# Optimization experiments

Measured on AMD Instinct MI355X. Metric: run time of the kernel, lower is better.

## Reference

```python
import jax, jax.numpy as jnp
import numpy as np

IMG = 1280
STRIDES = (8, 16, 32)
ALPHA, GAMMA = 0.25, 2.0
OBJ_W, BOX_W, FOOT_W = 1.0, 5.0, 1.0
RADIUS, NUM_CAND, EPS = 2.5, 10, 1e-7


def _grid(H, W):
    ys, xs = jnp.meshgrid(jnp.arange(H, dtype=jnp.float32),
                          jnp.arange(W, dtype=jnp.float32), indexing='ij')
    return xs.reshape(-1), ys.reshape(-1)


def _iou_xyxy(a, b):
    lt = jnp.maximum(a[..., :2], b[..., :2])
    rb = jnp.minimum(a[..., 2:], b[..., 2:])
    wh = jnp.clip(rb - lt, 0.0)
    inter = wh[..., 0] * wh[..., 1]
    aa = (a[..., 2] - a[..., 0]) * (a[..., 3] - a[..., 1])
    ab = (b[..., 2] - b[..., 0]) * (b[..., 3] - b[..., 1])
    return inter / (aa + ab - inter + EPS)


def _assign_one(pred, gt_boxes, gt_foots, gt_valid, stride):
    # Faithful SimOTAAssigner.assign for one image/scale (torch @no_grad).
    pred = jax.lax.stop_gradient(pred)
    gt_boxes = jax.lax.stop_gradient(gt_boxes)
    gt_foots = jax.lax.stop_gradient(gt_foots)
    C, H, W = pred.shape
    HW = H * W
    gx, gy = _grid(H, W)
    s = stride / IMG
    p = pred.reshape(C, HW)
    obj_logit = p[0]
    pcx = (jax.nn.sigmoid(p[1]) + gx) * s
    pcy = (jax.nn.sigmoid(p[2]) + gy) * s
    pw = jnp.exp(jnp.clip(p[3], -5.0, 5.0)) * s
    ph = jnp.exp(jnp.clip(p[4], -5.0, 5.0)) * s
    pred_xyxy = jnp.stack([pcx - pw / 2, pcy - ph / 2, pcx + pw / 2, pcy + ph / 2], -1)
    cls_cost = jax.nn.softplus(-obj_logit)  # BCE_with_logits(logit, 1)
    cell = jnp.arange(HW)

    def step(carry, gt):
        obj_t, box_t, foot_t, pos_m = carry
        box, foot, valid = gt
        cx, cy, w, h = box[0], box[1], box[2], box[3]
        cxg, cyg = cx / s, cy / s
        in_center = (jnp.abs(gx - cxg) < RADIUS) & (jnp.abs(gy - cyg) < RADIUS)
        in_box = ((gx >= (cx - w / 2) / s) & (gx < (cx + w / 2) / s) &
                  (gy >= (cy - h / 2) / s) & (gy < (cy + h / 2) / s))
        cand = in_center | in_box
        dist = (gx - cxg) ** 2 + (gy - cyg) ** 2
        cand = jnp.where(jnp.any(cand), cand, cell == jnp.argmin(dist))
        gt_xyxy = jnp.stack([cx - w / 2, cy - h / 2, cx + w / 2, cy + h / 2])
        iou = _iou_xyxy(pred_xyxy, gt_xyxy)  # (HW,)
        cost = jnp.where(cand, cls_cost - 3.0 * jnp.log(iou + EPS), jnp.inf)
        n_cand = jnp.sum(cand)
        iou_sum = jnp.sum(jnp.where(cand, iou, 0.0))
        n_pos = jnp.clip(jnp.floor(iou_sum).astype(jnp.int32), 1,
                         jnp.minimum(NUM_CAND, n_cand))
        _, idx = jax.lax.top_k(-cost, NUM_CAND)
        sel = (jnp.arange(NUM_CAND) < n_pos) & valid
        best_iou = iou[idx[0]]  # pair_iou[topk_idx[0]] in the torch code
        pos_m = pos_m.at[idx].max(sel.astype(jnp.float32))
        obj_t = obj_t.at[idx].max(jnp.where(sel, best_iou, -jnp.inf))
        tx = cxg - gx[idx]
        ty = cyg - gy[idx]
        tw = jnp.log(w / s + EPS)
        th = jnp.log(h / s + EPS)
        new_box = jnp.stack([tx, ty, jnp.full_like(tx, tw), jnp.full_like(tx, th)], 0)
        box_t = box_t.at[:, idx].set(jnp.where(sel, new_box, box_t[:, idx]))
        new_foot = jnp.stack([jnp.full_like(tx, foot[0]), jnp.full_like(tx, foot[1])], 0)
        foot_t = foot_t.at[:, idx].set(jnp.where(sel, new_foot, foot_t[:, idx]))
        return (obj_t, box_t, foot_t, pos_m), None

    init = (jnp.zeros(HW), jnp.zeros((4, HW)), jnp.zeros((2, HW)), jnp.zeros(HW))
    (obj_t, box_t, foot_t, pos_m), _ = jax.lax.scan(
        step, init, (gt_boxes, gt_foots, gt_valid))
    return obj_t, box_t, foot_t, pos_m


def _ciou(pcx, pcy, pw, ph, tcx, tcy, tw, th):
    px1, py1, px2, py2 = pcx - pw / 2, pcy - ph / 2, pcx + pw / 2, pcy + ph / 2
    tx1, ty1, tx2, ty2 = tcx - tw / 2, tcy - th / 2, tcx + tw / 2, tcy + th / 2
    iw = jnp.clip(jnp.minimum(px2, tx2) - jnp.maximum(px1, tx1), 0.0)
    ih = jnp.clip(jnp.minimum(py2, ty2) - jnp.maximum(py1, ty1), 0.0)
    inter = iw * ih
    union = pw * ph + tw * th - inter + EPS
    iou = inter / union
    rho2 = (pcx - tcx) ** 2 + (pcy - tcy) ** 2
    cw = jnp.maximum(px2, tx2) - jnp.minimum(px1, tx1)
    ch = jnp.maximum(py2, ty2) - jnp.minimum(py1, ty1)
    c2 = cw ** 2 + ch ** 2 + EPS
    v = (4.0 / jnp.pi ** 2) * (jnp.arctan(tw / (th + EPS)) - jnp.arctan(pw / (ph + EPS))) ** 2
    alpha = jax.lax.stop_gradient(v / (1.0 - iou + v + EPS))
    return iou - rho2 / c2 - alpha * v


def _loss_one(pred, gt_boxes, gt_foots, gt_valid, stride):
    obj_t, box_t, foot_t, pm = _assign_one(pred, gt_boxes, gt_foots, gt_valid, stride)
    C, H, W = pred.shape
    HW = H * W
    p = pred.reshape(C, HW)
    gx, gy = _grid(H, W)
    s = stride / IMG
    # focal loss on objectness with soft IoU targets
    x, z = p[0], obj_t
    ce = jnp.maximum(x, 0.0) - x * z + jnp.log1p(jnp.exp(-jnp.abs(x)))
    prob = jax.nn.sigmoid(x)
    p_t = prob * z + (1.0 - prob) * (1.0 - z)
    a_t = ALPHA * z + (1.0 - ALPHA) * (1.0 - z)
    obj_loss = jnp.mean(a_t * (1.0 - p_t) ** GAMMA * ce)
    npos = jnp.maximum(jnp.sum(pm), 1.0)
    # CIoU box loss at positive cells (mask instead of gather, jit-friendly)
    pcx = (jax.nn.sigmoid(p[1]) + gx) * s
    pcy = (jax.nn.sigmoid(p[2]) + gy) * s
    pw = jnp.exp(jnp.clip(p[3], -5.0, 5.0)) * s
    ph = jnp.exp(jnp.clip(p[4], -5.0, 5.0)) * s
    tcx = (box_t[0] + gx) * s
    tcy = (box_t[1] + gy) * s
    tw = jnp.exp(box_t[2]) * s
    th = jnp.exp(box_t[3]) * s
    ciou = _ciou(pcx, pcy, pw, ph, tcx, tcy, tw, th)
    box_loss = jnp.sum(pm * (1.0 - ciou)) / npos
    # smooth-L1 foot loss on sigmoid-decoded foot point
    pf = jax.nn.sigmoid(p[5:7])
    d = jnp.abs(pf - foot_t)
    sl1 = jnp.where(d < 1.0, 0.5 * d * d, d - 0.5)
    foot_loss = jnp.sum(pm * jnp.sum(sl1, 0)) / npos
    return obj_loss, box_loss, foot_loss


def _forward(pred_s0, pred_s1, pred_s2, targets):
    B = pred_s0.shape[0]
    person = targets[..., 0] == 0  # person_mask; padded rows use cls != 0
    boxes = targets[..., 1:5]
    foots = targets[..., 5:7]
    size = jnp.maximum(boxes[..., 2], boxes[..., 3]) * IMG
    scale_masks = (size < 128.0, (size >= 48.0) & (size < 288.0), size >= 128.0)
    tot_obj = tot_box = tot_foot = 0.0
    for pred, stride, sm in zip((pred_s0, pred_s1, pred_s2), STRIDES, scale_masks):
        valid = person & sm
        o, bx, f = jax.vmap(_loss_one, in_axes=(0, 0, 0, 0, None))(
            pred, boxes, foots, valid, stride)
        tot_obj = tot_obj + jnp.sum(o)
        tot_box = tot_box + jnp.sum(bx)
        tot_foot = tot_foot + jnp.sum(f)
    return (OBJ_W * tot_obj + BOX_W * tot_box + FOOT_W * tot_foot) / B


def setup_inputs() -> dict:
    key = jax.random.key(0)
    ks = jax.random.split(key, 7)
    B, N = 64, 40
    pred_s0 = jax.random.normal(ks[0], (B, 7, 160, 160), jnp.float32)
    pred_s1 = jax.random.normal(ks[1], (B, 7, 80, 80), jnp.float32)
    pred_s2 = jax.random.normal(ks[2], (B, 7, 40, 40), jnp.float32)
    cls = (jax.random.uniform(ks[3], (B, N, 1)) > 0.9).astype(jnp.float32)
    cxy = jax.random.uniform(ks[4], (B, N, 2)) * 0.8 + 0.1
    wh = jax.random.uniform(ks[5], (B, N, 2)) * 0.28 + 0.01
    ft = jax.random.uniform(ks[6], (B, N, 2))
    targets = jnp.concatenate([cls, cxy, wh, ft], -1)
    return {"pred_s0": pred_s0, "pred_s1": pred_s1, "pred_s2": pred_s2,
            "targets": targets}


def reference(pred_s0, pred_s1, pred_s2, targets):
    return _forward(pred_s0, pred_s1, pred_s2, targets)
```

## Files before the change

### kernel.cpp

```cpp
#include <hip/hip_runtime.h>
#include <math.h>

#define NBATCH 64
#define NGT    40
#define HW0    25600
#define HW1    6400
#define HW2    1600
#define NTASK  (NBATCH*3*NGT)
#define SLICE  1600
#define BPB    21
#define NBLK   (NBATCH*BPB)
#define SENT   0xFFFFFFFFFFFFFFFFull
#define FEPS   1e-7f

__device__ __forceinline__ float sigm(float x){ return 1.0f/(1.0f+expf(-x)); }

__device__ __forceinline__ unsigned fkey(float f){
  unsigned b = __float_as_uint(f);
  return (b & 0x80000000u) ? ~b : (b | 0x80000000u);
}

__device__ __forceinline__ unsigned long long shflx64(unsigned long long v, int m){
  int lo = __shfl_xor((int)(unsigned)(v & 0xFFFFFFFFull), m, 64);
  int hi = __shfl_xor((int)(unsigned)(v >> 32), m, 64);
  return (((unsigned long long)(unsigned)hi) << 32) | (unsigned)lo;
}
__device__ __forceinline__ float wredf(float v){
  #pragma unroll
  for (int o=32;o;o>>=1) v += __shfl_xor(v,o,64);
  return v;
}
__device__ __forceinline__ int wredi(int v){
  #pragma unroll
  for (int o=32;o;o>>=1) v += __shfl_xor(v,o,64);
  return v;
}
__device__ __forceinline__ unsigned long long wredmin64(unsigned long long v){
  #pragma unroll
  for (int o=32;o;o>>=1){ unsigned long long w = shflx64(v,o); v = (w<v)?w:v; }
  return v;
}

__device__ __forceinline__ float iou_of_cell(const float* __restrict__ P, int HW, int cell,
                                             int W, float s,
                                             float bx1, float by1, float bx2, float by2, float ab){
  int gy = cell / W;
  int gx = cell - gy*W;
  float gxf=(float)gx, gyf=(float)gy;
  float q1 = P[HW+cell], q2=P[2*HW+cell], q3=P[3*HW+cell], q4=P[4*HW+cell];
  float pcx = (sigm(q1)+gxf)*s;
  float pcy = (sigm(q2)+gyf)*s;
  float pw = expf(fminf(fmaxf(q3,-5.0f),5.0f))*s;
  float ph = expf(fminf(fmaxf(q4,-5.0f),5.0f))*s;
  float ax1=pcx-pw*0.5f, ay1=pcy-ph*0.5f, ax2=pcx+pw*0.5f, ay2=pcy+ph*0.5f;
  float ltx=fmaxf(ax1,bx1), lty=fmaxf(ay1,by1);
  float rbx=fminf(ax2,bx2), rby=fminf(ay2,by2);
  float iw=fmaxf(rbx-ltx,0.0f), ih=fmaxf(rby-lty,0.0f);
  float inter=iw*ih;
  float aa=(ax2-ax1)*(ay2-ay1);
  return inter/(aa+ab-inter+FEPS);
}

__global__ __launch_bounds__(256) void k_assign(
    const float* __restrict__ p0, const float* __restrict__ p1,
    const float* __restrict__ p2, const float* __restrict__ tg,
    int2* __restrict__ meta, int* __restrict__ cells)
{
  int lane = threadIdx.x & 63;
  int task = ((blockIdx.x<<8) + threadIdx.x) >> 6;
  int g  = task % NGT;
  int bs = task / NGT;
  int sc = bs % 3;
  int b  = bs / 3;

  const float* tp = tg + (b*NGT + g)*7;
  float cls = tp[0], cx = tp[1], cy = tp[2], w = tp[3], h = tp[4];
  float sz = fmaxf(w,h)*1280.0f;
  bool valid = (cls == 0.0f);
  if (sc==0)      valid = valid && (sz < 128.0f);
  else if (sc==1) valid = valid && (sz >= 48.0f) && (sz < 288.0f);
  else            valid = valid && (sz >= 128.0f);
  if (!valid){ if (lane==0) meta[task] = make_int2(0,0); return; }

  int W, HW; float s; const float* P;
  if (sc==0)      { W=160; HW=HW0; s=8.0f/1280.0f;  P=p0; }
  else if (sc==1) { W=80;  HW=HW1; s=16.0f/1280.0f; P=p1; }
  else            { W=40;  HW=HW2; s=32.0f/1280.0f; P=p2; }
  P += (size_t)b*7*HW;

  float cxg = cx/s, cyg = cy/s;
  float bx1 = cx - w*0.5f, bx2 = cx + w*0.5f;
  float by1 = cy - h*0.5f, by2 = cy + h*0.5f;
  float ab  = (bx2-bx1)*(by2-by1);
  float bxl = bx1/s, bxr = bx2/s, byt = by1/s, byb = by2/s;

  int x0 = max(0,   (int)floorf(fminf(cxg-2.5f, bxl)) - 1);
  int x1 = min(W-1, (int)floorf(fmaxf(cxg+2.5f, bxr)) + 1);
  int y0 = max(0,   (int)floorf(fminf(cyg-2.5f, byt)) - 1);
  int y1 = min(W-1, (int)floorf(fmaxf(cyg+2.5f, byb)) + 1);
  int rw = x1-x0+1, rh = y1-y0+1;
  int rn = rw*rh;

  unsigned long long t[10];
  #pragma unroll
  for (int j=0;j<10;++j) t[j]=SENT;
  int ncand = 0; float iousum = 0.0f;
  unsigned long long dmin = SENT;

  int rx = lane % rw, ry = lane / rw;
  int stepy = 64 / rw, stepx = 64 % rw;
  for (int r = lane; r < rn; r += 64){
    float gxf = (float)(x0+rx), gyf = (float)(y0+ry);
    int cell = (y0+ry)*W + (x0+rx);
    float q1 = P[HW+cell], q2 = P[2*HW+cell], q3 = P[3*HW+cell], q4 = P[4*HW+cell];
    float pcx = (sigm(q1)+gxf)*s;
    float pcy = (sigm(q2)+gyf)*s;
    float pw = expf(fminf(fmaxf(q3,-5.0f),5.0f))*s;
    float ph = expf(fminf(fmaxf(q4,-5.0f),5.0f))*s;
    float ax1 = pcx-pw*0.5f, ay1 = pcy-ph*0.5f, ax2 = pcx+pw*0.5f, ay2 = pcy+ph*0.5f;
    float ltx = fmaxf(ax1,bx1), lty = fmaxf(ay1,by1);
    float rbx = fminf(ax2,bx2), rby = fminf(ay2,by2);
    float iw = fmaxf(rbx-ltx,0.0f), ih = fmaxf(rby-lty,0.0f);
    float inter = iw*ih;
    float aa = (ax2-ax1)*(ay2-ay1);
    float iou = inter/(aa+ab-inter+FEPS);
    bool ic = (fabsf(gxf-cxg)<2.5f) && (fabsf(gyf-cyg)<2.5f);
    bool ib = (gxf>=bxl)&&(gxf<bxr)&&(gyf>=byt)&&(gyf<byb);
    float dx = gxf-cxg, dy = gyf-cyg;
    float dist = dx*dx+dy*dy;
    unsigned long long dk = (((unsigned long long)__float_as_uint(dist))<<32)|(unsigned)cell;
    dmin = (dk<dmin)?dk:dmin;
    if (ic|ib){
      ncand += 1; iousum += iou;
      float q0 = P[cell];
      float ccost = fmaxf(-q0,0.0f) + log1pf(expf(-fabsf(q0)));
      float cost = ccost - 3.0f*logf(iou+FEPS);
      unsigned long long pk = (((unsigned long long)fkey(cost))<<32)|(unsigned)cell;
      if (pk < t[9]){
        t[9] = pk;
        #pragma unroll
        for (int j=9;j>0;--j){ if (t[j]<t[j-1]){ unsigned long long tmp=t[j]; t[j]=t[j-1]; t[j-1]=tmp; } }
      }
    }
    rx += stepx; ry += stepy;
    if (rx >= rw){ rx -= rw; ry += 1; }
  }

  int NC = wredi(ncand);
  float IS = wredf(iousum);
  dmin = wredmin64(dmin);

  unsigned long long g10[10];
  int ptr = 0;
  #pragma unroll
  for (int rd=0; rd<10; ++rd){
    unsigned long long head = SENT;
    #pragma unroll
    for (int j=0;j<10;++j) head = (ptr==j)? t[j] : head;
    unsigned long long m = wredmin64(head);
    g10[rd] = m;
    if (head==m && m!=SENT) ptr += 1;
  }

  if (lane==0){
    unsigned cell0; int npos;
    if (NC==0){ cell0 = (unsigned)dmin; npos = 1; }
    else {
      cell0 = (unsigned)g10[0];
      int ub = NC < 10 ? NC : 10;
      int v = (int)floorf(IS);
      v = v < 1 ? 1 : v;
      npos = v > ub ? ub : v;
    }
    float biou = iou_of_cell(P, HW, (int)cell0, W, s, bx1, by1, bx2, by2, ab);
    meta[task] = make_int2(npos, __float_as_int(biou));
    #pragma unroll
    for (int sl=0; sl<10; ++sl){
      if (sl < npos) cells[task*10 + sl] = (int)((sl==0)? cell0 : (unsigned)g10[sl]);
    }
  }
}

template<int W, int HW>
__device__ __forceinline__ void loss_slice(
    const float* __restrict__ P, const float* __restrict__ tg,
    int b, int off, float s,
    const float* __restrict__ s_obj, const int* __restrict__ s_win, float* acc)
{
  int tid = threadIdx.x;
  int i0 = off + tid;
  int gy = i0 / W;
  int gx = i0 - gy*W;
  const int SY = 320 / W;
  float xv[5];
  #pragma unroll
  for (int k=0;k<5;++k) xv[k] = P[i0 + k*320];
  #pragma unroll
  for (int k=0;k<5;++k){
    int j = tid + k*320;
    int i = off + j;
    float x = xv[k];
    float z = s_obj[j];
    float e = __expf(-fabsf(x));
    float ce = fmaxf(x,0.0f) - x*z + __logf(1.0f + e);
    float prob = 1.0f/(1.0f + __expf(-x));
    float p_t = prob*z + (1.0f-prob)*(1.0f-z);
    float a_t = 0.25f*z + 0.75f*(1.0f-z);
    float om = 1.0f - p_t;
    acc[0] += a_t*om*om*ce;
    int wg = s_win[j];
    if (wg >= 0){
      acc[1] += 1.0f;
      const float* tp = tg + (b*NGT + wg)*7;
      float cx=tp[1], cy=tp[2], w=tp[3], h=tp[4], fx=tp[5], fy=tp[6];
      float gxf=(float)gx, gyf=(float)gy;
      float pcx = (1.0f/(1.0f+__expf(-P[HW+i]))+gxf)*s;
      float pcy = (1.0f/(1.0f+__expf(-P[2*HW+i]))+gyf)*s;
      float pw = __expf(fminf(fmaxf(P[3*HW+i],-5.0f),5.0f))*s;
      float ph = __expf(fminf(fmaxf(P[4*HW+i],-5.0f),5.0f))*s;
      float tw = w + FEPS*s, th = h + FEPS*s;
      float px1=pcx-pw*0.5f, py1=pcy-ph*0.5f, px2=pcx+pw*0.5f, py2=pcy+ph*0.5f;
      float tx1=cx-tw*0.5f, ty1=cy-th*0.5f, tx2=cx+tw*0.5f, ty2=cy+th*0.5f;
      float iw = fmaxf(fminf(px2,tx2)-fmaxf(px1,tx1),0.0f);
      float ih = fmaxf(fminf(py2,ty2)-fmaxf(py1,ty1),0.0f);
      float inter = iw*ih;
      float uni = pw*ph + tw*th - inter + FEPS;
      float iou = inter/uni;
      float rho2 = (pcx-cx)*(pcx-cx)+(pcy-cy)*(pcy-cy);
      float cw = fmaxf(px2,tx2)-fminf(px1,tx1);
      float ch = fmaxf(py2,ty2)-fminf(py1,ty1);
      float c2 = cw*cw+ch*ch+FEPS;
      float da = atanf(tw/(th+FEPS)) - atanf(pw/(ph+FEPS));
      float v = (4.0f/(float)(M_PI*M_PI))*da*da;
      float alpha = v/(1.0f-iou+v+FEPS);
      float ciou = iou - rho2/c2 - alpha*v;
      acc[2] += 1.0f - ciou;
      float pf1 = 1.0f/(1.0f+__expf(-P[5*HW+i]));
      float pf2 = 1.0f/(1.0f+__expf(-P[6*HW+i]));
      float d1 = fabsf(pf1-fx), d2 = fabsf(pf2-fy);
      acc[3] += (d1<1.0f? 0.5f*d1*d1 : d1-0.5f) + (d2<1.0f? 0.5f*d2*d2 : d2-0.5f);
    }
    gy += SY;
  }
}

__global__ __launch_bounds__(320) void k_loss(
    const float* __restrict__ p0, const float* __restrict__ p1,
    const float* __restrict__ p2, const float* __restrict__ tg,
    const int2* __restrict__ meta, const int* __restrict__ cells,
    float* __restrict__ partials)
{
  __shared__ float s_obj[SLICE];
  __shared__ int   s_win[SLICE];
  __shared__ float red[4][5];

  int u = blockIdx.x;
  int b = u / BPB, r = u % BPB;
  int sc, off, HW; const float* P; float s;
  if (r < 16)      { sc=0; HW=HW0; s=8.0f/1280.0f;  off=r*SLICE;      P=p0; }
  else if (r < 20) { sc=1; HW=HW1; s=16.0f/1280.0f; off=(r-16)*SLICE; P=p1; }
  else             { sc=2; HW=HW2; s=32.0f/1280.0f; off=0;            P=p2; }
  P += (size_t)b*7*HW;

  for (int j = threadIdx.x; j < SLICE; j += 320){ s_obj[j]=0.0f; s_win[j]=-1; }
  __syncthreads();

  int tbase = (b*3 + sc)*NGT;
  for (int t = threadIdx.x; t < NGT*10; t += 320){
    int g = t / 10, sl = t % 10;
    int2 m = meta[tbase + g];
    if (sl < m.x){
      int l = cells[(tbase+g)*10 + sl] - off;
      if (l >= 0 && l < SLICE){
        atomicMax(&s_win[l], g);
        atomicMax((int*)(s_obj+l), m.y);
      }
    }
  }
  __syncthreads();

  float acc[4] = {0.0f,0.0f,0.0f,0.0f};
  if (sc==0)      loss_slice<160,HW0>(P, tg, b, off, s, s_obj, s_win, acc);
  else if (sc==1) loss_slice<80, HW1>(P, tg, b, off, s, s_obj, s_win, acc);
  else            loss_slice<40, HW2>(P, tg, b, off, s, s_obj, s_win, acc);

  int wv = threadIdx.x >> 6, lane = threadIdx.x & 63;
  #pragma unroll
  for (int q=0;q<4;++q) acc[q] = wredf(acc[q]);
  if (lane==0){ red[0][wv]=acc[0]; red[1][wv]=acc[1]; red[2][wv]=acc[2]; red[3][wv]=acc[3]; }
  __syncthreads();
  if (threadIdx.x==0){
    float a0=0,a1=0,a2=0,a3=0;
    #pragma unroll
    for (int j=0;j<5;++j){ a0+=red[0][j]; a1+=red[1][j]; a2+=red[2][j]; a3+=red[3][j]; }
    partials[u*4+0]=a0; partials[u*4+1]=a1; partials[u*4+2]=a2; partials[u*4+3]=a3;
  }
}

__global__ void k_final(const float* __restrict__ partials, float* __restrict__ out){
  int t = threadIdx.x;
  float c = 0.0f;
  if (t < 192){
    int b = t/3, sc = t%3;
    float os=0,np=0,bs=0,fs=0;
    int base = b*BPB;
    int r0, r1;
    if (sc==0){ r0=0; r1=16; }
    else if (sc==1){ r0=16; r1=20; }
    else { r0=20; r1=21; }
    for (int j=r0;j<r1;++j){
      const float* q = partials + (base+j)*4;
      os+=q[0]; np+=q[1]; bs+=q[2]; fs+=q[3];
    }
    float hw = (sc==0)?25600.0f:(sc==1)?6400.0f:1600.0f;
    float npos = fmaxf(np, 1.0f);
    c = os/hw + 5.0f*bs/npos + fs/npos;
  }
  __shared__ float sh[256];
  sh[t] = c;
  __syncthreads();
  for (int s2=128; s2>0; s2>>=1){
    if (t < s2) sh[t] += sh[t+s2];
    __syncthreads();
  }
  if (t==0) out[0] = sh[0]*(1.0f/64.0f);
}

extern "C" void kernel_launch(void* const* d_in, const int* in_sizes, int n_in,
                              void* d_out, int out_size, void* d_ws, size_t ws_size,
                              hipStream_t stream) {
  (void)in_sizes; (void)n_in; (void)out_size; (void)ws_size;
  const float* p0 = (const float*)d_in[0];
  const float* p1 = (const float*)d_in[1];
  const float* p2 = (const float*)d_in[2];
  const float* tg = (const float*)d_in[3];

  int2*  meta     = (int2*)d_ws;
  int*   cells    = (int*)((char*)d_ws + (size_t)NTASK*8);
  float* partials = (float*)((char*)d_ws + (size_t)NTASK*8 + (size_t)NTASK*40);
  float* out      = (float*)d_out;

  k_assign<<<NTASK/4, 256, 0, stream>>>(p0, p1, p2, tg, meta, cells);
  k_loss  <<<NBLK, 320, 0, stream>>>(p0, p1, p2, tg, meta, cells, partials);
  k_final <<<1, 256, 0, stream>>>(partials, out);
}
```

Before: 128.3 us.

## Fuse final reduction into loss kernel via atomics and use fast math intrinsics

The separate final-reduction kernel is removed. Each loss block now atomically adds its partial sums into per-(batch, scale) slots and bumps a completion counter, and the last block computes the scalar output. The slots and counter are zeroed inside the assign kernel. The exact sigmoid, exp, log and divide calls in the assign and loss kernels are also swapped for hardware reciprocal and fast exp/log intrinsics. This saves one kernel launch and some transcendental cost, but float atomics make the summation order nondeterministic and the fast intrinsics lower precision, which could change the top-k candidate ordering.

```diff
diff --git a/kernel.cpp b/kernel.cpp
--- a/kernel.cpp
+++ b/kernel.cpp
@@ -13,6 +13,8 @@
 #define SENT   0xFFFFFFFFFFFFFFFFull
 #define FEPS   1e-7f
 
+__device__ __forceinline__ float frcp(float x){ return __builtin_amdgcn_rcpf(x); }
+__device__ __forceinline__ float fsigm(float x){ return frcp(1.0f + __expf(-x)); }
 __device__ __forceinline__ float sigm(float x){ return 1.0f/(1.0f+expf(-x)); }
 
 __device__ __forceinline__ unsigned fkey(float f){
@@ -64,8 +66,13 @@
 __global__ __launch_bounds__(256) void k_assign(
     const float* __restrict__ p0, const float* __restrict__ p1,
     const float* __restrict__ p2, const float* __restrict__ tg,
-    int2* __restrict__ meta, int* __restrict__ cells)
+    int2* __restrict__ meta, int* __restrict__ cells,
+    float* __restrict__ slots, int* __restrict__ counter)
 {
+  if (blockIdx.x == 0){
+    for (int j = threadIdx.x; j < 192*4; j += 256) slots[j] = 0.0f;
+    if (threadIdx.x == 0) *counter = 0;
+  }
   int lane = threadIdx.x & 63;
   int task = ((blockIdx.x<<8) + threadIdx.x) >> 6;
   int g  = task % NGT;
@@ -88,11 +95,12 @@
   else            { W=40;  HW=HW2; s=32.0f/1280.0f; P=p2; }
   P += (size_t)b*7*HW;
 
-  float cxg = cx/s, cyg = cy/s;
+  float inv_s = 1280.0f/(float)((sc==0)?8:(sc==1)?16:32);
+  float cxg = cx*inv_s, cyg = cy*inv_s;
   float bx1 = cx - w*0.5f, bx2 = cx + w*0.5f;
   float by1 = cy - h*0.5f, by2 = cy + h*0.5f;
   float ab  = (bx2-bx1)*(by2-by1);
-  float bxl = bx1/s, bxr = bx2/s, byt = by1/s, byb = by2/s;
+  float bxl = bx1*inv_s, bxr = bx2*inv_s, byt = by1*inv_s, byb = by2*inv_s;
 
   int x0 = max(0,   (int)floorf(fminf(cxg-2.5f, bxl)) - 1);
   int x1 = min(W-1, (int)floorf(fmaxf(cxg+2.5f, bxr)) + 1);
@@ -113,17 +121,17 @@
     float gxf = (float)(x0+rx), gyf = (float)(y0+ry);
     int cell = (y0+ry)*W + (x0+rx);
     float q1 = P[HW+cell], q2 = P[2*HW+cell], q3 = P[3*HW+cell], q4 = P[4*HW+cell];
-    float pcx = (sigm(q1)+gxf)*s;
-    float pcy = (sigm(q2)+gyf)*s;
-    float pw = expf(fminf(fmaxf(q3,-5.0f),5.0f))*s;
-    float ph = expf(fminf(fmaxf(q4,-5.0f),5.0f))*s;
+    float pcx = (fsigm(q1)+gxf)*s;
+    float pcy = (fsigm(q2)+gyf)*s;
+    float pw = __expf(fminf(fmaxf(q3,-5.0f),5.0f))*s;
+    float ph = __expf(fminf(fmaxf(q4,-5.0f),5.0f))*s;
     float ax1 = pcx-pw*0.5f, ay1 = pcy-ph*0.5f, ax2 = pcx+pw*0.5f, ay2 = pcy+ph*0.5f;
     float ltx = fmaxf(ax1,bx1), lty = fmaxf(ay1,by1);
     float rbx = fminf(ax2,bx2), rby = fminf(ay2,by2);
     float iw = fmaxf(rbx-ltx,0.0f), ih = fmaxf(rby-lty,0.0f);
     float inter = iw*ih;
     float aa = (ax2-ax1)*(ay2-ay1);
-    float iou = inter/(aa+ab-inter+FEPS);
+    float iou = inter * frcp(aa+ab-inter+FEPS);
     bool ic = (fabsf(gxf-cxg)<2.5f) && (fabsf(gyf-cyg)<2.5f);
     bool ib = (gxf>=bxl)&&(gxf<bxr)&&(gyf>=byt)&&(gyf<byb);
     float dx = gxf-cxg, dy = gyf-cyg;
@@ -133,8 +141,8 @@
     if (ic|ib){
       ncand += 1; iousum += iou;
       float q0 = P[cell];
-      float ccost = fmaxf(-q0,0.0f) + log1pf(expf(-fabsf(q0)));
-      float cost = ccost - 3.0f*logf(iou+FEPS);
+      float ccost = fmaxf(-q0,0.0f) + __logf(1.0f + __expf(-fabsf(q0)));
+      float cost = ccost - 3.0f*__logf(iou+FEPS);
       unsigned long long pk = (((unsigned long long)fkey(cost))<<32)|(unsigned)cell;
       if (pk < t[9]){
         t[9] = pk;
@@ -203,7 +211,7 @@
     float z = s_obj[j];
     float e = __expf(-fabsf(x));
     float ce = fmaxf(x,0.0f) - x*z + __logf(1.0f + e);
-    float prob = 1.0f/(1.0f + __expf(-x));
+    float prob = frcp(1.0f + __expf(-x));
     float p_t = prob*z + (1.0f-prob)*(1.0f-z);
     float a_t = 0.25f*z + 0.75f*(1.0f-z);
     float om = 1.0f - p_t;
@@ -214,8 +222,8 @@
       const float* tp = tg + (b*NGT + wg)*7;
       float cx=tp[1], cy=tp[2], w=tp[3], h=tp[4], fx=tp[5], fy=tp[6];
       float gxf=(float)gx, gyf=(float)gy;
-      float pcx = (1.0f/(1.0f+__expf(-P[HW+i]))+gxf)*s;
-      float pcy = (1.0f/(1.0f+__expf(-P[2*HW+i]))+gyf)*s;
+      float pcx = (fsigm(P[HW+i])+gxf)*s;
+      float pcy = (fsigm(P[2*HW+i])+gyf)*s;
       float pw = __expf(fminf(fmaxf(P[3*HW+i],-5.0f),5.0f))*s;
       float ph = __expf(fminf(fmaxf(P[4*HW+i],-5.0f),5.0f))*s;
       float tw = w + FEPS*s, th = h + FEPS*s;
@@ -235,8 +243,8 @@
       float alpha = v/(1.0f-iou+v+FEPS);
       float ciou = iou - rho2/c2 - alpha*v;
       acc[2] += 1.0f - ciou;
-      float pf1 = 1.0f/(1.0f+__expf(-P[5*HW+i]));
-      float pf2 = 1.0f/(1.0f+__expf(-P[6*HW+i]));
+      float pf1 = fsigm(P[5*HW+i]);
+      float pf2 = fsigm(P[6*HW+i]);
       float d1 = fabsf(pf1-fx), d2 = fabsf(pf2-fy);
       acc[3] += (d1<1.0f? 0.5f*d1*d1 : d1-0.5f) + (d2<1.0f? 0.5f*d2*d2 : d2-0.5f);
     }
@@ -248,11 +256,13 @@
     const float* __restrict__ p0, const float* __restrict__ p1,
     const float* __restrict__ p2, const float* __restrict__ tg,
     const int2* __restrict__ meta, const int* __restrict__ cells,
-    float* __restrict__ partials)
+    float* __restrict__ slots, int* __restrict__ counter,
+    float* __restrict__ out)
 {
   __shared__ float s_obj[SLICE];
   __shared__ int   s_win[SLICE];
   __shared__ float red[4][5];
+  __shared__ int   s_done;
 
   int u = blockIdx.x;
   int b = u / BPB, r = u % BPB;
@@ -293,37 +303,40 @@
     float a0=0,a1=0,a2=0,a3=0;
     #pragma unroll
     for (int j=0;j<5;++j){ a0+=red[0][j]; a1+=red[1][j]; a2+=red[2][j]; a3+=red[3][j]; }
-    partials[u*4+0]=a0; partials[u*4+1]=a1; partials[u*4+2]=a2; partials[u*4+3]=a3;
-  }
-}
-
-__global__ void k_final(const float* __restrict__ partials, float* __restrict__ out){
-  int t = threadIdx.x;
-  float c = 0.0f;
-  if (t < 192){
-    int b = t/3, sc = t%3;
-    float os=0,np=0,bs=0,fs=0;
-    int base = b*BPB;
-    int r0, r1;
-    if (sc==0){ r0=0; r1=16; }
-    else if (sc==1){ r0=16; r1=20; }
-    else { r0=20; r1=21; }
-    for (int j=r0;j<r1;++j){
-      const float* q = partials + (base+j)*4;
-      os+=q[0]; np+=q[1]; bs+=q[2]; fs+=q[3];
-    }
-    float hw = (sc==0)?25600.0f:(sc==1)?6400.0f:1600.0f;
-    float npos = fmaxf(np, 1.0f);
-    c = os/hw + 5.0f*bs/npos + fs/npos;
-  }
-  __shared__ float sh[256];
-  sh[t] = c;
+    int slot = b*3 + sc;
+    atomicAdd(&slots[slot*4+0], a0);
+    atomicAdd(&slots[slot*4+1], a1);
+    atomicAdd(&slots[slot*4+2], a2);
+    atomicAdd(&slots[slot*4+3], a3);
+    __threadfence();
+    int old = __hip_atomic_fetch_add(counter, 1, __ATOMIC_ACQ_REL, __HIP_MEMORY_SCOPE_AGENT);
+    s_done = (old == NBLK-1);
+  }
   __syncthreads();
-  for (int s2=128; s2>0; s2>>=1){
-    if (t < s2) sh[t] += sh[t+s2];
+
+  if (s_done){
+    float c = 0.0f;
+    int t = threadIdx.x;
+    if (t < 192){
+      int scl = t % 3;
+      float os = __hip_atomic_load(&slots[t*4+0], __ATOMIC_ACQUIRE, __HIP_MEMORY_SCOPE_AGENT);
+      float np = __hip_atomic_load(&slots[t*4+1], __ATOMIC_ACQUIRE, __HIP_MEMORY_SCOPE_AGENT);
+      float bs = __hip_atomic_load(&slots[t*4+2], __ATOMIC_ACQUIRE, __HIP_MEMORY_SCOPE_AGENT);
+      float fs = __hip_atomic_load(&slots[t*4+3], __ATOMIC_ACQUIRE, __HIP_MEMORY_SCOPE_AGENT);
+      float hw = (scl==0)?25600.0f:(scl==1)?6400.0f:1600.0f;
+      float npos = fmaxf(np, 1.0f);
+      c = os/hw + 5.0f*bs/npos + fs/npos;
+    }
+    c = wredf(c);
+    if (lane==0) red[0][wv] = c;
     __syncthreads();
-  }
-  if (t==0) out[0] = sh[0]*(1.0f/64.0f);
+    if (threadIdx.x==0){
+      float a0=0;
+      #pragma unroll
+      for (int j=0;j<5;++j) a0 += red[0][j];
+      out[0] = a0*(1.0f/64.0f);
+    }
+  }
 }
 
 extern "C" void kernel_launch(void* const* d_in, const int* in_sizes, int n_in,
@@ -335,12 +348,12 @@
   const float* p2 = (const float*)d_in[2];
   const float* tg = (const float*)d_in[3];
 
-  int2*  meta     = (int2*)d_ws;
-  int*   cells    = (int*)((char*)d_ws + (size_t)NTASK*8);
-  float* partials = (float*)((char*)d_ws + (size_t)NTASK*8 + (size_t)NTASK*40);
-  float* out      = (float*)d_out;
-
-  k_assign<<<NTASK/4, 256, 0, stream>>>(p0, p1, p2, tg, meta, cells);
-  k_loss  <<<NBLK, 320, 0, stream>>>(p0, p1, p2, tg, meta, cells, partials);
-  k_final <<<1, 256, 0, stream>>>(partials, out);
-}
+  int2*  meta    = (int2*)d_ws;
+  int*   cells   = (int*)((char*)d_ws + (size_t)NTASK*8);
+  float* slots   = (float*)((char*)d_ws + (size_t)NTASK*48);
+  int*   counter = (int*)((char*)d_ws + (size_t)NTASK*48 + 192*4*4);
+  float* out     = (float*)d_out;
+
+  k_assign<<<NTASK/4, 256, 0, stream>>>(p0, p1, p2, tg, meta, cells, slots, counter);
+  k_loss  <<<NBLK, 320, 0, stream>>>(p0, p1, p2, tg, meta, cells, slots, counter, out);
+}
```

Measured after the change: 161.5 us. 1.26x slower.
